# Kernel optimization log

Measured on AMD Instinct MI355X. Metric: run time of the kernel, lower is better.

The kernel has to match this reference:

```python
import jax, jax.numpy as jnp
import numpy as np

N_HEADS = 16


def setup_inputs() -> dict:
    key = jax.random.key(0)
    k1, k2, k3 = jax.random.split(key, 3)
    n_embed = 1024
    b, t = 4, 2048
    x = jax.random.normal(k1, (b, t, n_embed), dtype=jnp.float32)
    # Linear weights stored as [in, out]; y = x @ W + b (same math as torch Linear).
    Wqkv = jax.random.normal(k2, (n_embed, 3 * n_embed), dtype=jnp.float32) * (n_embed ** -0.5)
    bqkv = jnp.zeros((3 * n_embed,), dtype=jnp.float32)
    Wout = jax.random.normal(k3, (n_embed, n_embed), dtype=jnp.float32) * (n_embed ** -0.5)
    bout = jnp.zeros((n_embed,), dtype=jnp.float32)
    return {"x": x, "Wqkv": Wqkv, "bqkv": bqkv, "Wout": Wout, "bout": bout}


def reference(x, Wqkv, bqkv, Wout, bout):
    b, t, n_embed = x.shape
    hs = n_embed // N_HEADS
    qkv = x @ Wqkv + bqkv  # [b, t, 3*n_embed]
    q, k, v = jnp.split(qkv, 3, axis=-1)
    # b t (h hs) -> b h t hs
    def to_heads(u):
        return u.reshape(b, t, N_HEADS, hs).transpose(0, 2, 1, 3)
    q, k, v = to_heads(q), to_heads(k), to_heads(v)
    scale = 1.0 / jnp.sqrt(jnp.asarray(hs, dtype=x.dtype))
    scores = jnp.einsum('bhqd,bhkd->bhqk', q, k) * scale  # [b, h, t, t]
    causal = jnp.tril(jnp.ones((t, t), dtype=bool))
    scores = jnp.where(causal, scores, jnp.finfo(scores.dtype).min)
    attn = jax.nn.softmax(scores, axis=-1)
    out = jnp.einsum('bhqk,bhkd->bhqd', attn, v)  # [b, h, t, hs]
    out = out.transpose(0, 2, 1, 3).reshape(b, t, n_embed)  # b h t hs -> b t (h hs)
    return out @ Wout + bout
```

## Files before the change

kernel.cpp:

```cpp
#include <hip/hip_runtime.h>
#include <hip/hip_bf16.h>
#include <stdint.h>

typedef unsigned short u16;
typedef __bf16 bf16x8 __attribute__((ext_vector_type(8)));
typedef float f32x4 __attribute__((ext_vector_type(4)));
typedef u16 ushort8 __attribute__((ext_vector_type(8)));
typedef short short4v __attribute__((ext_vector_type(4)));

__device__ __forceinline__ u16 f2bf(float f) {
    unsigned int u = __builtin_bit_cast(unsigned int, f);
    u += 0x7fffu + ((u >> 16) & 1u);
    return (u16)(u >> 16);
}

__device__ __forceinline__ unsigned pk2(float a, float b) {
    __hip_bfloat162 h = __float22bfloat162_rn(float2{a, b});
    unsigned u;
    __builtin_memcpy(&u, &h, 4);
    return u;
}

#define MFMA16(a, b, c) __builtin_amdgcn_mfma_f32_16x16x32_bf16( \
    __builtin_bit_cast(bf16x8, a), __builtin_bit_cast(bf16x8, b), c, 0, 0, 0)

#if defined(__has_builtin)
#if __has_builtin(__builtin_amdgcn_exp2f)
#define EXP2(x) __builtin_amdgcn_exp2f(x)
#endif
#endif
#ifndef EXP2
#define EXP2(x) __expf((x) * 0.69314718f)
#endif

__device__ __forceinline__ void async16(void* lds, const void* g) {
    __builtin_amdgcn_global_load_lds(
        (const __attribute__((address_space(1))) unsigned int*)(uintptr_t)g,
        (__attribute__((address_space(3))) unsigned int*)(unsigned int)(uintptr_t)lds,
        16, 0, 0);
}

__global__ __launch_bounds__(256) void convert_bf16(
    const float* __restrict__ src, u16* __restrict__ dst)
{
    int i = blockIdx.x * 256 + threadIdx.x;
    float4 f0 = ((const float4*)src)[i * 2];
    float4 f1 = ((const float4*)src)[i * 2 + 1];
    ushort8 v;
    v[0]=f2bf(f0.x); v[1]=f2bf(f0.y); v[2]=f2bf(f0.z); v[3]=f2bf(f0.w);
    v[4]=f2bf(f1.x); v[5]=f2bf(f1.y); v[6]=f2bf(f1.z); v[7]=f2bf(f1.w);
    ((ushort8*)dst)[i] = v;
}

__global__ __launch_bounds__(256) void transpose_convert(
    const float* __restrict__ src, u16* __restrict__ dst, int N, int K)
{
    __shared__ u16 T[64][68];
    const int k0 = blockIdx.x * 64, n0 = blockIdx.y * 64;
    const int tid = threadIdx.x;
    const int rr = tid >> 4, cc = (tid & 15) * 4;
    #pragma unroll
    for (int rnd = 0; rnd < 4; ++rnd) {
        int r = rr + rnd * 16;
        float4 f = *(const float4*)&src[(size_t)(k0 + r) * N + n0 + cc];
        u16 v[4] = {f2bf(f.x), f2bf(f.y), f2bf(f.z), f2bf(f.w)};
        *(unsigned long long*)&T[r][cc] = *(unsigned long long*)v;
    }
    __syncthreads();
    #pragma unroll
    for (int rnd = 0; rnd < 4; ++rnd) {
        int rn = rr + rnd * 16;
        u16 v[4];
        #pragma unroll
        for (int j = 0; j < 4; ++j) v[j] = T[cc + j][rn];
        *(unsigned long long*)&dst[(size_t)(n0 + rn) * K + k0 + cc] =
            *(unsigned long long*)v;
    }
}

#define NT32 32
#define BUF32 16384

__device__ __forceinline__ void stage32(
    const u16* __restrict__ A, const u16* __restrict__ Bt,
    u16* Lb, int m0, int n0, int k0, int w, int lane)
{
    const int rbl = lane >> 5;
    const int chunk = (lane >> 3) & 3;
    const int row = lane & 7;
    #pragma unroll
    for (int r = 0; r < 2; ++r) {
        int rb = w * 4 + r * 2 + rbl;
        async16(Lb + (w * 4 + r * 2) * 256,
                A + (size_t)(m0 + rb * 8 + row) * 1024 + k0 + chunk * 8);
    }
    #pragma unroll
    for (int r = 0; r < 2; ++r) {
        int rb = w * 4 + r * 2 + rbl;
        async16(Lb + 8192 + (w * 4 + r * 2) * 256,
                Bt + (size_t)(n0 + rb * 8 + row) * 1024 + k0 + chunk * 8);
    }
}

__device__ __forceinline__ void gemm_mainloop32(
    const u16* __restrict__ A, const u16* __restrict__ Bt,
    u16* L, int m0, int n0, int tid, f32x4 acc[8][4])
{
    const int lane = tid & 63, w = tid >> 6;
    const int lr = lane & 15, quad = lane >> 4;
    const int wm = w >> 2, wn = w & 3;
    const int arb = wm * 16 + (lr >> 3);
    const int brb = wn * 8 + (lr >> 3);
    const int foff = quad * 64 + (lr & 7) * 8;

    stage32(A, Bt, L, m0, n0, 0, w, lane);
    asm volatile("s_waitcnt vmcnt(0)" ::: "memory");
    __builtin_amdgcn_s_barrier();
    asm volatile("" ::: "memory");

    #pragma unroll 2
    for (int t = 0; t < NT32; ++t) {
        const u16* As = L + (t & 1) * BUF32;
        const u16* Bs = As + 8192;

        if (t + 1 < NT32) {
            stage32(A, Bt, L + ((t + 1) & 1) * BUF32, m0, n0, (t + 1) * 32,
                    w, lane);
            asm volatile("s_waitcnt vmcnt(4)" ::: "memory");
        } else {
            asm volatile("s_waitcnt vmcnt(0)" ::: "memory");
        }
        __builtin_amdgcn_s_barrier();
        asm volatile("" ::: "memory");

        ushort8 b[4], a03[4], a47[4];
        #pragma unroll
        for (int nt = 0; nt < 4; ++nt)
            b[nt] = *(const ushort8*)&Bs[(brb + nt * 2) * 256 + foff];
        #pragma unroll
        for (int mt = 0; mt < 4; ++mt)
            a03[mt] = *(const ushort8*)&As[(arb + mt * 2) * 256 + foff];
        __builtin_amdgcn_sched_barrier(0);
        #pragma unroll
        for (int mt = 0; mt < 4; ++mt)
            a47[mt] = *(const ushort8*)&As[(arb + (mt + 4) * 2) * 256 + foff];
        asm volatile("s_waitcnt lgkmcnt(4)" ::: "memory");
        __builtin_amdgcn_sched_barrier(0);
        __builtin_amdgcn_s_setprio(1);
        #pragma unroll
        for (int mt = 0; mt < 4; ++mt)
            #pragma unroll
            for (int nt = 0; nt < 4; ++nt)
                acc[mt][nt] = MFMA16(a03[mt], b[nt], acc[mt][nt]);
        __builtin_amdgcn_s_setprio(0);
        asm volatile("s_waitcnt lgkmcnt(0)" ::: "memory");
        __builtin_amdgcn_sched_barrier(0);
        __builtin_amdgcn_s_setprio(1);
        #pragma unroll
        for (int mt = 0; mt < 4; ++mt)
            #pragma unroll
            for (int nt = 0; nt < 4; ++nt)
                acc[mt + 4][nt] = MFMA16(a47[mt], b[nt], acc[mt + 4][nt]);
        __builtin_amdgcn_s_setprio(0);
        __builtin_amdgcn_s_barrier();
        asm volatile("" ::: "memory");
    }
}

__global__ __launch_bounds__(512, 2) void qkv_gemm(
    const u16* __restrict__ xb, const u16* __restrict__ Wt,
    const float* __restrict__ bias, u16* __restrict__ qkvb)
{
    __shared__ u16 L[2 * BUF32];
    const int m0 = blockIdx.x * 256, n0 = blockIdx.y * 256;
    const int tid = threadIdx.x;
    f32x4 acc[8][4] = {};
    gemm_mainloop32(xb, Wt, L, m0, n0, tid, acc);

    const int lane = tid & 63, w = tid >> 6;
    const int lr = lane & 15, quad = lane >> 4;
    const int wm = w >> 2, wn = w & 3;
    const int which = n0 >> 10;
    float bv[4];
    #pragma unroll
    for (int nt = 0; nt < 4; ++nt) bv[nt] = bias[n0 + wn * 64 + nt * 16 + lr];

    if (which == 2) {
        u16* vT = qkvb + (size_t)2 * 8388608;
        #pragma unroll
        for (int nt = 0; nt < 4; ++nt) {
            int n = n0 + wn * 64 + nt * 16 + lr;
            int hh = (n >> 6) & 15, d = n & 63;
            #pragma unroll
            for (int mt = 0; mt < 8; ++mt) {
                int mbase = m0 + wm * 128 + mt * 16 + quad * 4;
                int b_idx = mbase >> 11, t0 = mbase & 2047;
                short4v o4;
                #pragma unroll
                for (int reg = 0; reg < 4; ++reg)
                    o4[reg] = (short)f2bf(acc[mt][nt][reg] + bv[nt]);
                *(short4v*)&vT[((size_t)(b_idx * 16 + hh) * 64 + d) * 2048 + t0] = o4;
            }
        }
    } else {
        u16* dst = qkvb + (size_t)which * 8388608;
        #pragma unroll
        for (int mt = 0; mt < 8; ++mt)
          #pragma unroll
          for (int nt = 0; nt < 4; ++nt) {
            int n = n0 + wn * 64 + nt * 16 + lr;
            int hh = (n >> 6) & 15, d = n & 63;
            #pragma unroll
            for (int reg = 0; reg < 4; ++reg) {
                int m = m0 + wm * 128 + mt * 16 + quad * 4 + reg;
                int b_idx = m >> 11, t_idx = m & 2047;
                dst[(((size_t)(b_idx * 16 + hh) * 2048 + t_idx) << 6) + d] =
                    f2bf(acc[mt][nt][reg] + bv[nt]);
            }
          }
    }
}

#define KT16 16

__device__ __forceinline__ void stage_tile256(
    const u16* __restrict__ A, const u16* __restrict__ Bt,
    u16* Lb, int m0, int n0, int k0, int w, int grow, int gchunk)
{
    #pragma unroll
    for (int r = 0; r < 4; ++r) {
        int rb = w * 4 + r;
        async16(Lb + rb * 512,
                A + (size_t)(m0 + rb * 8 + grow) * 1024 + k0 + gchunk * 8);
    }
    #pragma unroll
    for (int r = 0; r < 2; ++r) {
        int rb = w * 2 + r;
        async16(Lb + 16384 + rb * 512,
                Bt + (size_t)(n0 + rb * 8 + grow) * 1024 + k0 + gchunk * 8);
    }
}

__device__ __forceinline__ void gemm_mainloop256(
    const u16* __restrict__ A, const u16* __restrict__ Bt,
    u16* L, int m0, int n0, int tid, f32x4 acc[4][4])
{
    const int lane = tid & 63, w = tid >> 6;
    const int lr = lane & 15, quad = lane >> 4;
    const int wm = w >> 1, wn = w & 1;
    const int grow = lane & 7, gchunk = lane >> 3;

    stage_tile256(A, Bt, L,         m0, n0, 0,  w, grow, gchunk);
    stage_tile256(A, Bt, L + 24576, m0, n0, 64, w, grow, gchunk);

    u16* Lc = L;
    u16* Ls = L + 49152;
    u16* const Lend = L + 73728;

    for (int t = 0; t < KT16; ++t) {
        if (t < KT16 - 2)
            stage_tile256(A, Bt, Ls, m0, n0, (t + 2) * 64, w, grow, gchunk);

        if (t < KT16 - 2)       asm volatile("s_waitcnt vmcnt(12)" ::: "memory");
        else if (t == KT16 - 2) asm volatile("s_waitcnt vmcnt(6)"  ::: "memory");
        else                    asm volatile("s_waitcnt vmcnt(0)"  ::: "memory");
        __builtin_amdgcn_s_barrier();
        asm volatile("" ::: "memory");

        const u16* As = Lc;
        const u16* Bs = Lc + 16384;
        __builtin_amdgcn_s_setprio(1);
        #pragma unroll
        for (int kk = 0; kk < 2; ++kk) {
            ushort8 a[4], b[4];
            #pragma unroll
            for (int mt = 0; mt < 4; ++mt) {
                int rb = wm * 8 + mt * 2 + (lr >> 3);
                a[mt] = *(const ushort8*)&As[rb * 512 + (kk * 4 + quad) * 64 + (lr & 7) * 8];
            }
            #pragma unroll
            for (int nt = 0; nt < 4; ++nt) {
                int rb = wn * 8 + nt * 2 + (lr >> 3);
                b[nt] = *(const ushort8*)&Bs[rb * 512 + (kk * 4 + quad) * 64 + (lr & 7) * 8];
            }
            #pragma unroll
            for (int mt = 0; mt < 4; ++mt)
                #pragma unroll
                for (int nt = 0; nt < 4; ++nt)
                    acc[mt][nt] = MFMA16(a[mt], b[nt], acc[mt][nt]);
        }
        __builtin_amdgcn_s_setprio(0);
        asm volatile("" ::: "memory");
        __builtin_amdgcn_s_barrier();
        asm volatile("" ::: "memory");

        Lc += 24576; if (Lc == Lend) Lc = L;
        Ls += 24576; if (Ls == Lend) Ls = L;
    }
}

__global__ __launch_bounds__(512, 2) void out_gemm(
    const u16* __restrict__ A, const u16* __restrict__ Wt,
    const float* __restrict__ bias, float* __restrict__ out)
{
    __shared__ u16 L[73728];
    const int m0 = blockIdx.x * 256, n0 = blockIdx.y * 128;
    const int tid = threadIdx.x;
    f32x4 acc[4][4] = {};
    gemm_mainloop256(A, Wt, L, m0, n0, tid, acc);

    const int lane = tid & 63, w = tid >> 6;
    const int lr = lane & 15, quad = lane >> 4;
    const int wm = w >> 1, wn = w & 1;
    float bv[4];
    #pragma unroll
    for (int nt = 0; nt < 4; ++nt) bv[nt] = bias[n0 + wn * 64 + nt * 16 + lr];
    #pragma unroll
    for (int mt = 0; mt < 4; ++mt)
      #pragma unroll
      for (int nt = 0; nt < 4; ++nt)
        #pragma unroll
        for (int reg = 0; reg < 4; ++reg) {
            int m = m0 + wm * 64 + mt * 16 + quad * 4 + reg;
            int n = n0 + wn * 64 + nt * 16 + lr;
            out[(size_t)m * 1024 + n] = acc[mt][nt][reg] + bv[nt];
        }
}

__global__ __launch_bounds__(256) void attn_kernel(
    const u16* __restrict__ qkvb, u16* __restrict__ o_ws)
{
    const int orig = blockIdx.x + 16 * (blockIdx.y + 16 * blockIdx.z);
    const int work = (orig & 7) * 128 + (orig >> 3);
    const int p = work & 15, h = (work >> 4) & 15, b = work >> 8;
    const size_t bh = (size_t)(b * 16 + h) * 131072;
    const u16* Qb = qkvb + bh;
    const u16* Kb = qkvb + 8388608 + bh;
    const u16* Vt = qkvb + 2 * 8388608 + bh;
    __shared__ u16 Ks[2][4096];
    __shared__ u16 Vts[4096];
    __shared__ u16 Ps[64 * 72];
    const int tid = threadIdx.x, lane = tid & 63, w = tid >> 6;
    const int lr = lane & 15, quad = lane >> 4;
    const int grow = lane & 7, gchunk = lane >> 3;
    const float kscale = 0.125f * 1.44269504f;

    for (int pass = 0; pass < 2; ++pass) {
        const int qt = pass ? (31 - p) : p;
        ushort8 qf[2];
        {
            const u16* qr = Qb + (size_t)(qt * 64 + w * 16 + lr) * 64 + quad * 8;
            qf[0] = *(const ushort8*)qr;
            qf[1] = *(const ushort8*)(qr + 32);
        }
        f32x4 o_acc[4] = {};
        float m_i = -1e30f, l_i = 0.f;
        const int qrow = w * 16 + lr;
        const int bsrc = (lane & 48) + ((lane >> 4) << 2);

        __syncthreads();
        #pragma unroll
        for (int r = 0; r < 2; ++r) {
            int rb = w * 2 + r;
            async16(&Ks[0][rb * 512], Kb + (size_t)(rb * 8 + grow) * 64 + gchunk * 8);
        }

        for (int kt = 0; kt <= qt; ++kt) {
            const int buf = kt & 1;
            __syncthreads();

            #pragma unroll
            for (int r = 0; r < 2; ++r) {
                int rb = w * 2 + r;
                if (kt < qt)
                    async16(&Ks[buf ^ 1][rb * 512],
                            Kb + (size_t)((kt + 1) * 64 + rb * 8 + grow) * 64 + gchunk * 8);
                async16(&Vts[rb * 512],
                        Vt + (size_t)(rb * 8 + grow) * 2048 + kt * 64 + gchunk * 8);
            }

            f32x4 s[4] = {};
            #pragma unroll
            for (int nt = 0; nt < 4; ++nt)
                #pragma unroll
                for (int kk = 0; kk < 2; ++kk) {
                    ushort8 bb = *(ushort8*)&Ks[buf][(nt * 2 + (lr >> 3)) * 512 +
                                                     (kk * 4 + quad) * 64 + (lr & 7) * 8];
                    s[nt] = MFMA16(bb, qf[kk], s[nt]);
                }
            if (kt == qt) {
                #pragma unroll
                for (int nt = 0; nt < 4; ++nt)
                    #pragma unroll
                    for (int reg = 0; reg < 4; ++reg) {
                        int kc = nt * 16 + quad * 4 + reg;
                        if (kc > qrow) s[nt][reg] = -1e30f;
                    }
            }
            float mx = -1e30f;
            #pragma unroll
            for (int nt = 0; nt < 4; ++nt)
                #pragma unroll
                for (int reg = 0; reg < 4; ++reg) mx = fmaxf(mx, s[nt][reg]);
            mx = fmaxf(mx, __shfl_xor(mx, 16, 64));
            mx = fmaxf(mx, __shfl_xor(mx, 32, 64));
            float mxs = mx * kscale;
            if (!__all(mxs <= m_i + 8.0f)) {
                float mnew = fmaxf(m_i, mxs);
                float alpha = EXP2(m_i - mnew);
                m_i = mnew;
                l_i *= alpha;
                #pragma unroll
                for (int reg = 0; reg < 4; ++reg) {
                    float ar = __shfl(alpha, bsrc + reg, 64);
                    #pragma unroll
                    for (int dt = 0; dt < 4; ++dt) o_acc[dt][reg] *= ar;
                }
            }
            float p4[4][4];
            float rs = 0.f;
            #pragma unroll
            for (int nt = 0; nt < 4; ++nt)
                #pragma unroll
                for (int reg = 0; reg < 4; ++reg) {
                    float pv = EXP2(fmaf(s[nt][reg], kscale, -m_i));
                    p4[nt][reg] = pv;
                    rs += pv;
                }
            rs += __shfl_xor(rs, 16, 64);
            rs += __shfl_xor(rs, 32, 64);
            l_i += rs;
            #pragma unroll
            for (int nt = 0; nt < 4; ++nt) {
                unsigned lo = pk2(p4[nt][0], p4[nt][1]);
                unsigned hi = pk2(p4[nt][2], p4[nt][3]);
                unsigned long long pk = ((unsigned long long)hi << 32) | lo;
                *(unsigned long long*)&Ps[qrow * 72 + nt * 16 + quad * 4] = pk;
            }

            __syncthreads();

            #pragma unroll
            for (int kk = 0; kk < 2; ++kk) {
                ushort8 pa = *(ushort8*)&Ps[(w * 16 + lr) * 72 + kk * 32 + quad * 8];
                #pragma unroll
                for (int dt = 0; dt < 4; ++dt) {
                    ushort8 vb = *(ushort8*)&Vts[(dt * 2 + (lr >> 3)) * 512 +
                                                 (kk * 4 + quad) * 64 + (lr & 7) * 8];
                    o_acc[dt] = MFMA16(pa, vb, o_acc[dt]);
                }
            }
        }

        float rinv = 1.0f / l_i;
        float rl[4];
        #pragma unroll
        for (int reg = 0; reg < 4; ++reg) rl[reg] = __shfl(rinv, bsrc + reg, 64);
        #pragma unroll
        for (int dt = 0; dt < 4; ++dt)
            #pragma unroll
            for (int reg = 0; reg < 4; ++reg) {
                int row = w * 16 + quad * 4 + reg;
                int tq = qt * 64 + row;
                o_ws[((size_t)(b * 2048 + tq) << 10) + h * 64 + dt * 16 + lr] =
                    f2bf(o_acc[dt][reg] * rl[reg]);
            }
    }
}

extern "C" void kernel_launch(void* const* d_in, const int* in_sizes, int n_in,
                              void* d_out, int out_size, void* d_ws, size_t ws_size,
                              hipStream_t stream)
{
    const float* x    = (const float*)d_in[0];
    const float* Wqkv = (const float*)d_in[1];
    const float* bqkv = (const float*)d_in[2];
    const float* Wout = (const float*)d_in[3];
    const float* bout = (const float*)d_in[4];
    float* out = (float*)d_out;

    u16* qkvb = (u16*)d_ws;
    u16* xb   = qkvb + (size_t)3 * 8388608;
    u16* wT   = qkvb + (size_t)4 * 8388608;
    u16* attn_o = xb;

    convert_bf16<<<4096, 256, 0, stream>>>(x, xb);
    transpose_convert<<<dim3(16, 48), 256, 0, stream>>>(Wqkv, wT, 3072, 1024);
    qkv_gemm<<<dim3(32, 12), 512, 0, stream>>>(xb, wT, bqkv, qkvb);
    attn_kernel<<<dim3(16, 16, 4), 256, 0, stream>>>(qkvb, attn_o);
    transpose_convert<<<dim3(16, 16), 256, 0, stream>>>(Wout, wT, 1024, 1024);
    out_gemm<<<dim3(32, 8), 512, 0, stream>>>(attn_o, wT, bout, out);
}
```

Before: 271.8 us.

## Fuse both causal query tiles into one KV sweep sharing K/V loads

Instead of two sequential passes over key tiles for query tiles p and 31-p, the attention kernel now processes both query tiles in a single loop over key tiles. Each loaded K and V tile serves both query blocks while the shorter one is still active, which roughly halves K/V global traffic for the overlapped range and removes a pass of pipeline startup. The P scratch buffer is doubled and uses an XOR swizzle in place of padding to avoid LDS bank conflicts. The cost is higher register pressure from holding two sets of accumulators and softmax state.

```diff
diff --git a/kernel.cpp b/kernel.cpp
--- a/kernel.cpp
+++ b/kernel.cpp
@@ -325,6 +325,89 @@
             int n = n0 + wn * 64 + nt * 16 + lr;
             out[(size_t)m * 1024 + n] = acc[mt][nt][reg] + bv[nt];
         }
+}
+
+__device__ __forceinline__ void tile_qk_sm(
+    const u16* __restrict__ Ksb, const ushort8 qf[2], u16* __restrict__ PsT,
+    float& m_i, float& l_i, f32x4 o_acc[4],
+    bool diag, int lr, int quad, int qrow, int bsrc, float kscale)
+{
+    f32x4 s[4] = {};
+    #pragma unroll
+    for (int nt = 0; nt < 4; ++nt)
+        #pragma unroll
+        for (int kk = 0; kk < 2; ++kk) {
+            ushort8 bb = *(const ushort8*)&Ksb[(nt * 2 + (lr >> 3)) * 512 +
+                                               (kk * 4 + quad) * 64 + (lr & 7) * 8];
+            s[nt] = MFMA16(bb, qf[kk], s[nt]);
+        }
+    if (diag) {
+        #pragma unroll
+        for (int nt = 0; nt < 4; ++nt)
+            #pragma unroll
+            for (int reg = 0; reg < 4; ++reg) {
+                int kc = nt * 16 + quad * 4 + reg;
+                if (kc > qrow) s[nt][reg] = -1e30f;
+            }
+    }
+    float mx = -1e30f;
+    #pragma unroll
+    for (int nt = 0; nt < 4; ++nt)
+        #pragma unroll
+        for (int reg = 0; reg < 4; ++reg) mx = fmaxf(mx, s[nt][reg]);
+    mx = fmaxf(mx, __shfl_xor(mx, 16, 64));
+    mx = fmaxf(mx, __shfl_xor(mx, 32, 64));
+    float mxs = mx * kscale;
+    if (!__all(mxs <= m_i + 8.0f)) {
+        float mnew = fmaxf(m_i, mxs);
+        float alpha = EXP2(m_i - mnew);
+        m_i = mnew;
+        l_i *= alpha;
+        #pragma unroll
+        for (int reg = 0; reg < 4; ++reg) {
+            float ar = __shfl(alpha, bsrc + reg, 64);
+            #pragma unroll
+            for (int dt = 0; dt < 4; ++dt) o_acc[dt][reg] *= ar;
+        }
+    }
+    float p4[4][4];
+    float rs = 0.f;
+    #pragma unroll
+    for (int nt = 0; nt < 4; ++nt)
+        #pragma unroll
+        for (int reg = 0; reg < 4; ++reg) {
+            float pv = EXP2(fmaf(s[nt][reg], kscale, -m_i));
+            p4[nt][reg] = pv;
+            rs += pv;
+        }
+    rs += __shfl_xor(rs, 16, 64);
+    rs += __shfl_xor(rs, 32, 64);
+    l_i += rs;
+    const int swz = (qrow & 7) << 3;
+    #pragma unroll
+    for (int nt = 0; nt < 4; ++nt) {
+        unsigned lo = pk2(p4[nt][0], p4[nt][1]);
+        unsigned hi = pk2(p4[nt][2], p4[nt][3]);
+        unsigned long long pk = ((unsigned long long)hi << 32) | lo;
+        *(unsigned long long*)&PsT[qrow * 64 + ((nt * 16 + quad * 4) ^ swz)] = pk;
+    }
+}
+
+__device__ __forceinline__ void tile_pv(
+    const u16* __restrict__ Vtsb, const u16* __restrict__ PsT,
+    f32x4 o_acc[4], int lr, int quad, int qrow)
+{
+    const int swz = (qrow & 7) << 3;
+    #pragma unroll
+    for (int kk = 0; kk < 2; ++kk) {
+        ushort8 pa = *(const ushort8*)&PsT[qrow * 64 + ((kk * 32 + quad * 8) ^ swz)];
+        #pragma unroll
+        for (int dt = 0; dt < 4; ++dt) {
+            ushort8 vb = *(const ushort8*)&Vtsb[(dt * 2 + (lr >> 3)) * 512 +
+                                                (kk * 4 + quad) * 64 + (lr & 7) * 8];
+            o_acc[dt] = MFMA16(pa, vb, o_acc[dt]);
+        }
+    }
 }
 
 __global__ __launch_bounds__(256) void attn_kernel(
@@ -339,120 +422,62 @@
     const u16* Vt = qkvb + 2 * 8388608 + bh;
     __shared__ u16 Ks[2][4096];
     __shared__ u16 Vts[4096];
-    __shared__ u16 Ps[64 * 72];
+    __shared__ u16 Ps[2][4096];
     const int tid = threadIdx.x, lane = tid & 63, w = tid >> 6;
     const int lr = lane & 15, quad = lane >> 4;
     const int grow = lane & 7, gchunk = lane >> 3;
     const float kscale = 0.125f * 1.44269504f;
 
-    for (int pass = 0; pass < 2; ++pass) {
-        const int qt = pass ? (31 - p) : p;
-        ushort8 qf[2];
-        {
-            const u16* qr = Qb + (size_t)(qt * 64 + w * 16 + lr) * 64 + quad * 8;
-            qf[0] = *(const ushort8*)qr;
-            qf[1] = *(const ushort8*)(qr + 32);
-        }
-        f32x4 o_acc[4] = {};
-        float m_i = -1e30f, l_i = 0.f;
-        const int qrow = w * 16 + lr;
-        const int bsrc = (lane & 48) + ((lane >> 4) << 2);
-
+    const int qA = 31 - p, qB = p;
+    ushort8 qfA[2], qfB[2];
+    {
+        const u16* qra = Qb + (size_t)(qA * 64 + w * 16 + lr) * 64 + quad * 8;
+        qfA[0] = *(const ushort8*)qra;
+        qfA[1] = *(const ushort8*)(qra + 32);
+        const u16* qrb = Qb + (size_t)(qB * 64 + w * 16 + lr) * 64 + quad * 8;
+        qfB[0] = *(const ushort8*)qrb;
+        qfB[1] = *(const ushort8*)(qrb + 32);
+    }
+    f32x4 oA[4] = {}, oB[4] = {};
+    float mA = -1e30f, lA = 0.f, mB = -1e30f, lB = 0.f;
+    const int qrow = w * 16 + lr;
+    const int bsrc = (lane & 48) + ((lane >> 4) << 2);
+
+    #pragma unroll
+    for (int r = 0; r < 2; ++r) {
+        int rb = w * 2 + r;
+        async16(&Ks[0][rb * 512], Kb + (size_t)(rb * 8 + grow) * 64 + gchunk * 8);
+    }
+
+    for (int kt = 0; kt <= qA; ++kt) {
+        const int buf = kt & 1;
         __syncthreads();
+
         #pragma unroll
         for (int r = 0; r < 2; ++r) {
             int rb = w * 2 + r;
-            async16(&Ks[0][rb * 512], Kb + (size_t)(rb * 8 + grow) * 64 + gchunk * 8);
-        }
-
-        for (int kt = 0; kt <= qt; ++kt) {
-            const int buf = kt & 1;
-            __syncthreads();
-
-            #pragma unroll
-            for (int r = 0; r < 2; ++r) {
-                int rb = w * 2 + r;
-                if (kt < qt)
-                    async16(&Ks[buf ^ 1][rb * 512],
-                            Kb + (size_t)((kt + 1) * 64 + rb * 8 + grow) * 64 + gchunk * 8);
-                async16(&Vts[rb * 512],
-                        Vt + (size_t)(rb * 8 + grow) * 2048 + kt * 64 + gchunk * 8);
-            }
-
-            f32x4 s[4] = {};
-            #pragma unroll
-            for (int nt = 0; nt < 4; ++nt)
-                #pragma unroll
-                for (int kk = 0; kk < 2; ++kk) {
-                    ushort8 bb = *(ushort8*)&Ks[buf][(nt * 2 + (lr >> 3)) * 512 +
-                                                     (kk * 4 + quad) * 64 + (lr & 7) * 8];
-                    s[nt] = MFMA16(bb, qf[kk], s[nt]);
-                }
-            if (kt == qt) {
-                #pragma unroll
-                for (int nt = 0; nt < 4; ++nt)
-                    #pragma unroll
-                    for (int reg = 0; reg < 4; ++reg) {
-                        int kc = nt * 16 + quad * 4 + reg;
-                        if (kc > qrow) s[nt][reg] = -1e30f;
-                    }
-            }
-            float mx = -1e30f;
-            #pragma unroll
-            for (int nt = 0; nt < 4; ++nt)
-                #pragma unroll
-                for (int reg = 0; reg < 4; ++reg) mx = fmaxf(mx, s[nt][reg]);
-            mx = fmaxf(mx, __shfl_xor(mx, 16, 64));
-            mx = fmaxf(mx, __shfl_xor(mx, 32, 64));
-            float mxs = mx * kscale;
-            if (!__all(mxs <= m_i + 8.0f)) {
-                float mnew = fmaxf(m_i, mxs);
-                float alpha = EXP2(m_i - mnew);
-                m_i = mnew;
-                l_i *= alpha;
-                #pragma unroll
-                for (int reg = 0; reg < 4; ++reg) {
-                    float ar = __shfl(alpha, bsrc + reg, 64);
-                    #pragma unroll
-                    for (int dt = 0; dt < 4; ++dt) o_acc[dt][reg] *= ar;
-                }
-            }
-            float p4[4][4];
-            float rs = 0.f;
-            #pragma unroll
-            for (int nt = 0; nt < 4; ++nt)
-                #pragma unroll
-                for (int reg = 0; reg < 4; ++reg) {
-                    float pv = EXP2(fmaf(s[nt][reg], kscale, -m_i));
-                    p4[nt][reg] = pv;
-                    rs += pv;
-                }
-            rs += __shfl_xor(rs, 16, 64);
-            rs += __shfl_xor(rs, 32, 64);
-            l_i += rs;
-            #pragma unroll
-            for (int nt = 0; nt < 4; ++nt) {
-                unsigned lo = pk2(p4[nt][0], p4[nt][1]);
-                unsigned hi = pk2(p4[nt][2], p4[nt][3]);
-                unsigned long long pk = ((unsigned long long)hi << 32) | lo;
-                *(unsigned long long*)&Ps[qrow * 72 + nt * 16 + quad * 4] = pk;
-            }
-
-            __syncthreads();
-
-            #pragma unroll
-            for (int kk = 0; kk < 2; ++kk) {
-                ushort8 pa = *(ushort8*)&Ps[(w * 16 + lr) * 72 + kk * 32 + quad * 8];
-                #pragma unroll
-                for (int dt = 0; dt < 4; ++dt) {
-                    ushort8 vb = *(ushort8*)&Vts[(dt * 2 + (lr >> 3)) * 512 +
-                                                 (kk * 4 + quad) * 64 + (lr & 7) * 8];
-                    o_acc[dt] = MFMA16(pa, vb, o_acc[dt]);
-                }
-            }
-        }
-
-        float rinv = 1.0f / l_i;
+            if (kt < qA)
+                async16(&Ks[buf ^ 1][rb * 512],
+                        Kb + (size_t)((kt + 1) * 64 + rb * 8 + grow) * 64 + gchunk * 8);
+            async16(&Vts[rb * 512],
+                    Vt + (size_t)(rb * 8 + grow) * 2048 + kt * 64 + gchunk * 8);
+        }
+
+        tile_qk_sm(&Ks[buf][0], qfA, &Ps[0][0], mA, lA, oA,
+                   kt == qA, lr, quad, qrow, bsrc, kscale);
+        if (kt <= qB)
+            tile_qk_sm(&Ks[buf][0], qfB, &Ps[1][0], mB, lB, oB,
+                       kt == qB, lr, quad, qrow, bsrc, kscale);
+
+        __syncthreads();
+
+        tile_pv(Vts, &Ps[0][0], oA, lr, quad, qrow);
+        if (kt <= qB)
+            tile_pv(Vts, &Ps[1][0], oB, lr, quad, qrow);
+    }
+
+    {
+        float rinv = 1.0f / lA;
         float rl[4];
         #pragma unroll
         for (int reg = 0; reg < 4; ++reg) rl[reg] = __shfl(rinv, bsrc + reg, 64);
@@ -461,9 +486,24 @@
             #pragma unroll
             for (int reg = 0; reg < 4; ++reg) {
                 int row = w * 16 + quad * 4 + reg;
-                int tq = qt * 64 + row;
+                int tq = qA * 64 + row;
                 o_ws[((size_t)(b * 2048 + tq) << 10) + h * 64 + dt * 16 + lr] =
-                    f2bf(o_acc[dt][reg] * rl[reg]);
+                    f2bf(oA[dt][reg] * rl[reg]);
+            }
+    }
+    {
+        float rinv = 1.0f / lB;
+        float rl[4];
+        #pragma unroll
+        for (int reg = 0; reg < 4; ++reg) rl[reg] = __shfl(rinv, bsrc + reg, 64);
+        #pragma unroll
+        for (int dt = 0; dt < 4; ++dt)
+            #pragma unroll
+            for (int reg = 0; reg < 4; ++reg) {
+                int row = w * 16 + quad * 4 + reg;
+                int tq = qB * 64 + row;
+                o_ws[((size_t)(b * 2048 + tq) << 10) + h * 64 + dt * 16 + lr] =
+                    f2bf(oB[dt][reg] * rl[reg]);
             }
     }
 }
```

After: 283.9 us. 4.4% more time.
